# Kernel tuning notes

Hardware: AMD Instinct MI355X
Metric: run time of the kernel (lower is better)

The kernel has to match this reference:

```python
import jax, jax.numpy as jnp
import numpy as np
from math import pi

N_TRAJS, N_RES, N_BINS = 20, 300, 34
DIST_BIN_CENTRES = jnp.asarray(np.array([3.75 + 0.5 * i for i in range(N_BINS)], dtype=np.float32))
SIG = 1.25            # gauss_sigma
K_CB_DIST = 150.0
K_HB_DIST = 5.0
K_HB_GEN = 0.0
K_ANG_HB_GEN = 0.0
W_VIOL_MIN = 3.0      # weight_violate_min
EXP_MIN = 1.0         # pairwise_exponent_min
EXP_MAX = 0.75        # pairwise_exponent_max
HB_CUTOFF = 6.0       # hb_cutoff_gen
CUTOFF = 40.0         # pairwise_force_cutoff


def _norm(d):
    # safe euclidean norm over last axis (avoids NaN grad at exactly 0)
    return jnp.sqrt(jnp.maximum((d * d).sum(axis=-1), 1e-12))


def _safe_pow(x, p):
    pos = x > 0
    return jnp.where(pos, jnp.where(pos, x, 1.0) ** p, 0.0)


def _angle_forces(ba, bc, k, close, true_ang):
    ba_n = _norm(ba)
    bc_n = _norm(bc)
    cosang = jnp.clip((ba * bc).sum(-1) / jnp.clip(ba_n * bc_n, 0.1, 100.0), -1.0 + 1e-6, 1.0 - 1e-6)
    forces = k * close * (jnp.arccos(cosang) - true_ang)
    cr = jnp.cross(ba, bc)
    fa_vec = jnp.cross(-ba, cr)
    fc_vec = jnp.cross(bc, cr)
    fa = forces[..., None] * fa_vec / jnp.maximum(_norm(fa_vec), 0.1)[..., None]
    fc = forces[..., None] * fc_vec / jnp.maximum(_norm(fc_vec), 0.1)[..., None]
    fb = -fa - fc
    return fa, fb, fc


def setup_inputs() -> dict:
    key = jax.random.key(0)
    ks = jax.random.split(key, 9)
    B, R = N_TRAJS, N_RES
    base = jax.random.uniform(ks[0], (B, R, 3), dtype=jnp.float32) * 30.0
    def off(k):
        return base + jax.random.normal(k, (B, R, 3), dtype=jnp.float32)
    coords_N = off(ks[1]); coords_C = off(ks[2]); coords_O = off(ks[3])
    coords_CB = off(ks[4]); coords_H = off(ks[5])
    gaussian_weights = jax.random.normal(ks[6], (R, R, N_BINS), dtype=jnp.float32)
    hb_dists_min = 1.5 + 1.5 * jax.random.uniform(ks[7], (R, R), dtype=jnp.float32)
    hb_dists_max = hb_dists_min + 1.0 + 2.0 * jax.random.uniform(ks[8], (R, R), dtype=jnp.float32)
    return {"coords_N": coords_N, "coords_C": coords_C, "coords_O": coords_O,
            "coords_CB": coords_CB, "coords_H": coords_H,
            "gaussian_weights": gaussian_weights,
            "hb_dists_min": hb_dists_min, "hb_dists_max": hb_dists_max}


def reference(coords_N, coords_C, coords_O, coords_CB, coords_H,
              gaussian_weights, hb_dists_min, hb_dists_max):
    B, R, _ = coords_CB.shape
    idx = jnp.arange(R)
    # mask excluding |i-j| <= 2 (self and near-diagonal), as in the torch diag_mask
    diag_mask = (jnp.abs(idx[:, None] - idx[None, :]) > 2).astype(jnp.float32)[None]

    # --- CB distogram gaussian pairwise forces ---
    diffs_cb = coords_CB[:, None, :, :] - coords_CB[:, :, None, :]   # [B,i,j,3] = cb_j - cb_i
    dists_cb = jnp.clip(_norm(diffs_cb), 0.1, CUTOFF)                 # [B,i,j]
    norm_cb = diffs_cb / dists_cb[..., None]
    dfm = dists_cb[..., None] - DIST_BIN_CENTRES                      # [B,i,j,K]
    cb_e = gaussian_weights[None] * jnp.exp(-0.5 * (dfm / SIG) ** 2) / SIG
    f_cb = (-dfm / (SIG * SIG) * cb_e).sum(axis=3)                    # [B,i,j]
    pair_cb = -f_cb[..., None] * K_CB_DIST * norm_cb
    accs_CB = pair_cb.sum(axis=1)

    # --- H..O hydrogen-bond min/max distance restraints ---
    diffs_ho = coords_O[:, None, :, :] - coords_H[:, :, None, :]      # [B,i,j,3] = o_j - h_i
    dists_ho = jnp.clip(_norm(diffs_ho), 0.1, CUTOFF)
    norm_ho = diffs_ho / dists_ho[..., None]
    v_min = jnp.maximum(hb_dists_min[None] - dists_ho, 0.0)
    v_max = jnp.maximum(dists_ho - hb_dists_max[None], 0.0)
    close = (dists_ho < HB_CUTOFF).astype(jnp.float32) * diag_mask
    v_max_gen = close * jnp.maximum(dists_ho - HB_CUTOFF, 0.0)
    f_min = W_VIOL_MIN * K_HB_DIST * _safe_pow(v_min, EXP_MIN)
    f_max = K_HB_DIST * _safe_pow(v_max, EXP_MAX) + K_HB_GEN * _safe_pow(v_max_gen, EXP_MAX)
    pair_hb = (f_min - f_max)[..., None] * norm_ho
    accs_H = -pair_hb.sum(axis=2)
    accs_O = pair_hb.sum(axis=1)

    # --- O-H-N angle term (k_ang_hb_gen = 0, kept for fidelity) ---
    diffs_hn = (coords_N - coords_H)[:, :, None, :]                   # [B,i,1,3], broadcast over j
    fa, fb, fc = _angle_forces(diffs_ho, diffs_hn, K_ANG_HB_GEN, close, pi)
    accs_O = accs_O + fa.sum(axis=1)
    accs_H = accs_H + fb.sum(axis=2)
    accs_N = fc.sum(axis=2)

    # --- C-O-H angle term ---
    diffs_oc = (coords_C - coords_O)[:, :, None, :]                   # [B,i,1,3]
    fa2, fb2, fc2 = _angle_forces(diffs_oc, -diffs_ho, K_ANG_HB_GEN, close, pi)
    accs_C = fa2.sum(axis=2)
    accs_O = accs_O + fb2.sum(axis=1)
    accs_H = accs_H + fc2.sum(axis=2)

    return (accs_N, accs_C, accs_O, accs_CB, accs_H)
```

## Files before the change

### kernel.cpp

```cpp
#include <hip/hip_runtime.h>

#define NRES  300
#define NTRJ  20
#define NBINS 34
#define PLANE (NTRJ * NRES * 3)
#define IC    2
#define NCH   150
#define NHP   20
#define WROW  544
#define WF2   272
#define NRED  ((PLANE + 255) / 256)

#define EXP2F(x) __builtin_exp2f(x)
#define LOG2F(x) __builtin_log2f(x)

__device__ __forceinline__ float g16sum(float v) {
#pragma unroll
  for (int m = 1; m < 16; m <<= 1) v += __shfl_xor(v, m, 64);
  return v;
}

template <bool PART>
__global__ __launch_bounds__(256)
void force_fused(const float* __restrict__ cO, const float* __restrict__ cCB,
                 const float* __restrict__ cH, const float* __restrict__ gw,
                 const float* __restrict__ hmin, const float* __restrict__ hmax,
                 float* __restrict__ out, float* __restrict__ part) {
  __shared__ float wbuf[4][WROW];
  __shared__ float sCB[NTRJ * IC * 3];
  __shared__ float sHH[NTRJ * IC * 3];

  const int tid  = threadIdx.x;
  const int wv   = tid >> 6;
  const int lane = tid & 63;
  const int bsub = lane >> 4;
  const int jsub = lane & 15;
  const int jt   = blockIdx.x % 5;
  const int ch   = blockIdx.x / 5;
  const int i0   = ch * IC;
  const int j0w  = jt * 64 + wv * 16;
  const int j    = j0w + jsub;
  const bool jv  = (j < NRES);
  const int jc   = jv ? j : NRES - 1;
  const int nrow = min(16, max(0, NRES - j0w));
  const int E2   = nrow * 17;

  for (int e = tid; e < NTRJ * IC * 3; e += 256) {
    const int b = e / (IC * 3), r = e % (IC * 3);
    sCB[e] = cCB[((b * NRES) + i0 + r / 3) * 3 + (r % 3)];
    sHH[e] = cH [((b * NRES) + i0 + r / 3) * 3 + (r % 3)];
  }
  __syncthreads();

  float pjx[5], pjy[5], pjz[5], pox[5], poy[5], poz[5];
  float acx[5] = {}, acy[5] = {}, acz[5] = {};
  float aox[5] = {}, aoy[5] = {}, aoz[5] = {};
#pragma unroll
  for (int q = 0; q < 5; ++q) {
    const int b = bsub * 5 + q;
    const float* p = cCB + ((size_t)(b * NRES + jc)) * 3;
    pjx[q] = p[0]; pjy[q] = p[1]; pjz[q] = p[2];
    const float* o = cO + ((size_t)(b * NRES + jc)) * 3;
    pox[q] = o[0]; poy[q] = o[1]; poz[q] = o[2];
  }

  float2 r2[5];
  {
    const float2* src = (const float2*)gw + ((size_t)i0 * NRES + j0w) * 17;
#pragma unroll
    for (int u = 0; u < 5; ++u) {
      const int e = lane + u * 64;
      r2[u] = (e < E2) ? src[e] : make_float2(0.f, 0.f);
    }
  }

  float2* wd = (float2*)&wbuf[wv][0];
  for (int ii = 0; ii < IC; ++ii) {
    const int i = i0 + ii;
#pragma unroll
    for (int u = 0; u < 5; ++u) {
      const int e = lane + u * 64;
      if (e < WF2) wd[e] = r2[u];
    }
    if (ii + 1 < IC) {
      const float2* src =
          (const float2*)gw + ((size_t)(i + 1) * NRES + j0w) * 17;
#pragma unroll
      for (int u = 0; u < 5; ++u) {
        const int e = lane + u * 64;
        r2[u] = (e < E2) ? src[e] : make_float2(0.f, 0.f);
      }
    }

    float w[36];
    const float2* p2 = (const float2*)&wbuf[wv][jsub * NBINS];
#pragma unroll
    for (int k = 0; k < 17; ++k) { float2 v = p2[k]; w[2*k] = v.x; w[2*k+1] = v.y; }
    w[34] = 0.f; w[35] = 0.f;

    const float hmn = hmin[i * NRES + jc];
    const float hmx = hmax[i * NRES + jc];

#pragma unroll
    for (int q = 0; q < 5; ++q) {
      const int b = bsub * 5 + q;
      const float* pi = &sCB[(b * IC + ii) * 3];
      const float* ph = &sHH[(b * IC + ii) * 3];

      float dx = pjx[q] - pi[0], dy = pjy[q] - pi[1], dz = pjz[q] - pi[2];
      float d2 = fmaf(dx, dx, fmaf(dy, dy, dz * dz));
      d2 = fminf(fmaxf(d2, 0.01f), 1600.0f);
      float rinv = __frsqrt_rn(d2);
      float d    = d2 * rinv;
      float dA = d - 3.75f, dB = d - 9.75f, dC = d - 15.75f;
      float gA = EXP2F(-0.46166241f * dA * dA);
      float mA = EXP2F(fmaf(0.46166241f, dA, -0.11541560f));
      float gB = EXP2F(-0.46166241f * dB * dB);
      float mB = EXP2F(fmaf(0.46166241f, dB, -0.11541560f));
      float gC = EXP2F(-0.46166241f * dC * dC);
      float mC = EXP2F(fmaf(0.46166241f, dC, -0.11541560f));
      float s0 = 0.f, s1 = 0.f, s2 = 0.f;
#pragma unroll
      for (int k = 0; k < 12; ++k) {
        s0 = fmaf(w[k]      * dA, gA, s0); gA *= mA; mA *= 0.85214379f; dA -= 0.5f;
        s1 = fmaf(w[k + 12] * dB, gB, s1); gB *= mB; mB *= 0.85214379f; dB -= 0.5f;
        s2 = fmaf(w[k + 24] * dC, gC, s2); gC *= mC; mC *= 0.85214379f; dC -= 0.5f;
      }
      float cf = 76.8f * ((s0 + s1) + s2) * rinv;
      acx[q] = fmaf(cf, dx, acx[q]);
      acy[q] = fmaf(cf, dy, acy[q]);
      acz[q] = fmaf(cf, dz, acz[q]);

      float ex = pox[q] - ph[0], ey = poy[q] - ph[1], ez = poz[q] - ph[2];
      float e2 = fmaf(ex, ex, fmaf(ey, ey, ez * ez));
      e2 = fminf(fmaxf(e2, 0.01f), 1600.0f);
      float rh = __frsqrt_rn(e2);
      float dh = e2 * rh;
      float vmin = fmaxf(hmn - dh, 0.0f);
      float vmax = fmaxf(dh - hmx, 0.0f);
      float fmn = 15.0f * vmin;
      float fmx = (vmax > 0.0f) ? 5.0f * EXP2F(0.75f * LOG2F(vmax)) : 0.0f;
      float ff = (fmn - fmx) * rh;
      float qx = ff * ex, qy = ff * ey, qz = ff * ez;
      aox[q] += qx; aoy[q] += qy; aoz[q] += qz;

      float sx = g16sum(jv ? qx : 0.f);
      float sy = g16sum(jv ? qy : 0.f);
      float sz = g16sum(jv ? qz : 0.f);
      if (jsub == 0) {
        if constexpr (PART) {
          float* hp = part + ((size_t)(2 * NCH + jt * 4 + wv)) * PLANE +
                      ((size_t)b * NRES + i) * 3;
          hp[0] = -sx; hp[1] = -sy; hp[2] = -sz;
        } else {
          atomicAdd(&out[4 * PLANE + (b * NRES + i) * 3 + 0], -sx);
          atomicAdd(&out[4 * PLANE + (b * NRES + i) * 3 + 1], -sy);
          atomicAdd(&out[4 * PLANE + (b * NRES + i) * 3 + 2], -sz);
        }
      }
    }
  }

  if (jv) {
    if constexpr (PART) {
      float* pc  = part + (size_t)ch * PLANE;
      float* po2 = part + (size_t)(NCH + ch) * PLANE;
#pragma unroll
      for (int q = 0; q < 5; ++q) {
        const int base = ((bsub * 5 + q) * NRES + j) * 3;
        pc[base + 0]  = acx[q]; pc[base + 1]  = acy[q]; pc[base + 2]  = acz[q];
        po2[base + 0] = aox[q]; po2[base + 1] = aoy[q]; po2[base + 2] = aoz[q];
      }
    } else {
#pragma unroll
      for (int q = 0; q < 5; ++q) {
        const int base = ((bsub * 5 + q) * NRES + j) * 3;
        atomicAdd(&out[3 * PLANE + base + 0], acx[q]);
        atomicAdd(&out[3 * PLANE + base + 1], acy[q]);
        atomicAdd(&out[3 * PLANE + base + 2], acz[q]);
        atomicAdd(&out[2 * PLANE + base + 0], aox[q]);
        atomicAdd(&out[2 * PLANE + base + 1], aoy[q]);
        atomicAdd(&out[2 * PLANE + base + 2], aoz[q]);
      }
    }
  }
}

__global__ __launch_bounds__(256)
void reduce_seg(const float* __restrict__ part, float* __restrict__ out) {
  const int seg  = blockIdx.x / NRED;
  const int tblk = blockIdx.x % NRED;
  const int t    = tblk * 256 + threadIdx.x;
  if (t >= PLANE) return;

  int c0, cnt;
  float* dst;
  if (seg < 3)      { c0 = seg * 50;             cnt = 50; dst = out + 3 * PLANE; }
  else if (seg < 6) { c0 = NCH + (seg - 3) * 50; cnt = 50; dst = out + 2 * PLANE; }
  else              { c0 = 2 * NCH;              cnt = 20; dst = out + 4 * PLANE; }

  const float* p = part + t + (size_t)c0 * PLANE;
  float s[10] = {};
  for (int c = 0; c < cnt; c += 10) {
#pragma unroll
    for (int u = 0; u < 10; ++u) s[u] += p[(size_t)(c + u) * PLANE];
  }
  float tot = ((s[0] + s[1]) + (s[2] + s[3])) + ((s[4] + s[5]) + (s[6] + s[7])) +
              (s[8] + s[9]);
  atomicAdd(&dst[t], tot);
}

extern "C" void kernel_launch(void* const* d_in, const int* in_sizes, int n_in,
                              void* d_out, int out_size, void* d_ws, size_t ws_size,
                              hipStream_t stream) {
  const float* cO  = (const float*)d_in[2];
  const float* cCB = (const float*)d_in[3];
  const float* cH  = (const float*)d_in[4];
  const float* gw  = (const float*)d_in[5];
  const float* hmn = (const float*)d_in[6];
  const float* hmx = (const float*)d_in[7];
  float* out  = (float*)d_out;
  float* part = (float*)d_ws;

  const size_t need = (size_t)(2 * NCH + NHP) * PLANE * sizeof(float);

  (void)hipMemsetAsync(out, 0, (size_t)out_size * sizeof(float), stream);

  if (ws_size >= need) {
    force_fused<true><<<dim3(5 * NCH), dim3(256), 0, stream>>>(
        cO, cCB, cH, gw, hmn, hmx, out, part);
    reduce_seg<<<dim3(7 * NRED), dim3(256), 0, stream>>>(part, out);
  } else {
    force_fused<false><<<dim3(5 * NCH), dim3(256), 0, stream>>>(
        cO, cCB, cH, gw, hmn, hmx, out, nullptr);
  }
}
```

Baseline: 39.79 us.

## Split H-force accumulation into dedicated blocks, removing per-pair shuffle reductions

```diff
diff --git a/kernel.cpp b/kernel.cpp
--- a/kernel.cpp
+++ b/kernel.cpp
@@ -6,19 +6,16 @@
 #define PLANE (NTRJ * NRES * 3)
 #define IC    2
 #define NCH   150
-#define NHP   20
-#define WROW  544
-#define WF2   272
+#define NCBB  (5 * NCH)
+#define NHCH  15
+#define NHBB  (5 * NHCH)
+#define OFF_H (2 * NCH)
+#define NPLANES (2 * NCH + NHCH)
+#define WROWP 36
 #define NRED  ((PLANE + 255) / 256)
 
 #define EXP2F(x) __builtin_exp2f(x)
 #define LOG2F(x) __builtin_log2f(x)
-
-__device__ __forceinline__ float g16sum(float v) {
-#pragma unroll
-  for (int m = 1; m < 16; m <<= 1) v += __shfl_xor(v, m, 64);
-  return v;
-}
 
 template <bool PART>
 __global__ __launch_bounds__(256)
@@ -26,65 +23,51 @@
                  const float* __restrict__ cH, const float* __restrict__ gw,
                  const float* __restrict__ hmin, const float* __restrict__ hmax,
                  float* __restrict__ out, float* __restrict__ part) {
-  __shared__ float wbuf[4][WROW];
-  __shared__ float sCB[NTRJ * IC * 3];
-  __shared__ float sHH[NTRJ * IC * 3];
+  __shared__ __align__(16) float smem[3800];
 
   const int tid  = threadIdx.x;
   const int wv   = tid >> 6;
   const int lane = tid & 63;
-  const int bsub = lane >> 4;
-  const int jsub = lane & 15;
-  const int jt   = blockIdx.x % 5;
-  const int ch   = blockIdx.x / 5;
-  const int i0   = ch * IC;
-  const int j0w  = jt * 64 + wv * 16;
-  const int j    = j0w + jsub;
-  const bool jv  = (j < NRES);
-  const int jc   = jv ? j : NRES - 1;
-  const int nrow = min(16, max(0, NRES - j0w));
-  const int E2   = nrow * 17;
-
-  for (int e = tid; e < NTRJ * IC * 3; e += 256) {
-    const int b = e / (IC * 3), r = e % (IC * 3);
-    sCB[e] = cCB[((b * NRES) + i0 + r / 3) * 3 + (r % 3)];
-    sHH[e] = cH [((b * NRES) + i0 + r / 3) * 3 + (r % 3)];
-  }
-  __syncthreads();
-
-  float pjx[5], pjy[5], pjz[5], pox[5], poy[5], poz[5];
-  float acx[5] = {}, acy[5] = {}, acz[5] = {};
-  float aox[5] = {}, aoy[5] = {}, aoz[5] = {};
-#pragma unroll
-  for (int q = 0; q < 5; ++q) {
-    const int b = bsub * 5 + q;
-    const float* p = cCB + ((size_t)(b * NRES + jc)) * 3;
-    pjx[q] = p[0]; pjy[q] = p[1]; pjz[q] = p[2];
-    const float* o = cO + ((size_t)(b * NRES + jc)) * 3;
-    pox[q] = o[0]; poy[q] = o[1]; poz[q] = o[2];
-  }
-
-  float2 r2[5];
-  {
-    const float2* src = (const float2*)gw + ((size_t)i0 * NRES + j0w) * 17;
-#pragma unroll
-    for (int u = 0; u < 5; ++u) {
-      const int e = lane + u * 64;
-      r2[u] = (e < E2) ? src[e] : make_float2(0.f, 0.f);
-    }
-  }
-
-  float2* wd = (float2*)&wbuf[wv][0];
-  for (int ii = 0; ii < IC; ++ii) {
-    const int i = i0 + ii;
-#pragma unroll
-    for (int u = 0; u < 5; ++u) {
-      const int e = lane + u * 64;
-      if (e < WF2) wd[e] = r2[u];
-    }
-    if (ii + 1 < IC) {
-      const float2* src =
-          (const float2*)gw + ((size_t)(i + 1) * NRES + j0w) * 17;
+
+  if (blockIdx.x < NCBB) {
+    float* wbufw = smem + wv * (16 * WROWP);
+    float* sIC   = smem + 4 * (16 * WROWP);
+
+    const int bsub = lane >> 4;
+    const int jsub = lane & 15;
+    const int jt   = blockIdx.x % 5;
+    const int ch   = blockIdx.x / 5;
+    const int i0   = ch * IC;
+    const int j0w  = jt * 64 + wv * 16;
+    const int j    = j0w + jsub;
+    const bool jv  = (j < NRES);
+    const int jc   = jv ? j : NRES - 1;
+    const int E2   = 17 * min(16, max(0, NRES - j0w));
+
+    for (int e = tid; e < NTRJ * IC * 6; e += 256) {
+      const int b = e / (IC * 6), r = e % (IC * 6);
+      const int ii = r / 6, c = r % 6;
+      const int comp = (c < 3) ? c : c - 3;
+      const int src = ((b * NRES) + i0 + ii) * 3 + comp;
+      sIC[(b * IC + ii) * 8 + (c < 3 ? c : c + 1)] = (c < 3) ? cCB[src] : cH[src];
+    }
+    __syncthreads();
+
+    float pjx[5], pjy[5], pjz[5], pox[5], poy[5], poz[5];
+    float acx[5] = {}, acy[5] = {}, acz[5] = {};
+    float aox[5] = {}, aoy[5] = {}, aoz[5] = {};
+#pragma unroll
+    for (int q = 0; q < 5; ++q) {
+      const int b = bsub * 5 + q;
+      const float* p = cCB + ((size_t)(b * NRES + jc)) * 3;
+      pjx[q] = p[0]; pjy[q] = p[1]; pjz[q] = p[2];
+      const float* o = cO + ((size_t)(b * NRES + jc)) * 3;
+      pox[q] = o[0]; poy[q] = o[1]; poz[q] = o[2];
+    }
+
+    float2 r2[5];
+    {
+      const float2* src = (const float2*)gw + ((size_t)i0 * NRES + j0w) * 17;
 #pragma unroll
       for (int u = 0; u < 5; ++u) {
         const int e = lane + u * 64;
@@ -92,95 +75,181 @@
       }
     }
 
-    float w[36];
-    const float2* p2 = (const float2*)&wbuf[wv][jsub * NBINS];
-#pragma unroll
-    for (int k = 0; k < 17; ++k) { float2 v = p2[k]; w[2*k] = v.x; w[2*k+1] = v.y; }
-    w[34] = 0.f; w[35] = 0.f;
-
-    const float hmn = hmin[i * NRES + jc];
-    const float hmx = hmax[i * NRES + jc];
-
+    for (int ii = 0; ii < IC; ++ii) {
+      const int i = i0 + ii;
+#pragma unroll
+      for (int u = 0; u < 5; ++u) {
+        const int e = lane + u * 64;
+        if (e < 272) {
+          const int row = e / 17, col = e - row * 17;
+          ((float2*)wbufw)[row * 18 + col] = r2[u];
+        }
+      }
+      if (ii + 1 < IC) {
+        const float2* src =
+            (const float2*)gw + ((size_t)(i + 1) * NRES + j0w) * 17;
+#pragma unroll
+        for (int u = 0; u < 5; ++u) {
+          const int e = lane + u * 64;
+          r2[u] = (e < E2) ? src[e] : make_float2(0.f, 0.f);
+        }
+      }
+
+      float w[36];
+      {
+        const float4* wp = (const float4*)&wbufw[jsub * WROWP];
+#pragma unroll
+        for (int k4 = 0; k4 < 9; ++k4) {
+          float4 v = wp[k4];
+          w[4*k4+0] = v.x; w[4*k4+1] = v.y; w[4*k4+2] = v.z; w[4*k4+3] = v.w;
+        }
+        w[34] = 0.f; w[35] = 0.f;
+      }
+
+      const float hmn = hmin[i * NRES + jc];
+      const float hmx = hmax[i * NRES + jc];
+
+#pragma unroll
+      for (int q = 0; q < 5; ++q) {
+        const int b = bsub * 5 + q;
+        const float4* ic4 = (const float4*)&sIC[(b * IC + ii) * 8];
+        const float4 cb = ic4[0];
+        const float4 hh = ic4[1];
+
+        float dx = pjx[q] - cb.x, dy = pjy[q] - cb.y, dz = pjz[q] - cb.z;
+        float d2 = fmaf(dx, dx, fmaf(dy, dy, dz * dz));
+        d2 = fminf(fmaxf(d2, 0.01f), 1600.0f);
+        float rinv = __frsqrt_rn(d2);
+        float d    = d2 * rinv;
+        float dA = d - 3.75f, dB = d - 9.75f, dC = d - 15.75f;
+        float gA = EXP2F(-0.46166241f * dA * dA);
+        float mA = EXP2F(fmaf(0.46166241f, dA, -0.11541560f));
+        float gB = EXP2F(-0.46166241f * dB * dB);
+        float mB = EXP2F(fmaf(0.46166241f, dB, -0.11541560f));
+        float gC = EXP2F(-0.46166241f * dC * dC);
+        float mC = EXP2F(fmaf(0.46166241f, dC, -0.11541560f));
+        float s0 = 0.f, s1 = 0.f, s2 = 0.f;
+#pragma unroll
+        for (int k = 0; k < 12; ++k) {
+          s0 = fmaf(w[k]      * dA, gA, s0); gA *= mA; mA *= 0.85214379f; dA -= 0.5f;
+          s1 = fmaf(w[k + 12] * dB, gB, s1); gB *= mB; mB *= 0.85214379f; dB -= 0.5f;
+          s2 = fmaf(w[k + 24] * dC, gC, s2); gC *= mC; mC *= 0.85214379f; dC -= 0.5f;
+        }
+        float cf = 76.8f * ((s0 + s1) + s2) * rinv;
+        acx[q] = fmaf(cf, dx, acx[q]);
+        acy[q] = fmaf(cf, dy, acy[q]);
+        acz[q] = fmaf(cf, dz, acz[q]);
+
+        float ex = pox[q] - hh.x, ey = poy[q] - hh.y, ez = poz[q] - hh.z;
+        float e2 = fmaf(ex, ex, fmaf(ey, ey, ez * ez));
+        e2 = fminf(fmaxf(e2, 0.01f), 1600.0f);
+        float rh = __frsqrt_rn(e2);
+        float dh = e2 * rh;
+        float vmin = fmaxf(hmn - dh, 0.0f);
+        float vmax = fmaxf(dh - hmx, 0.0f);
+        float fmn = 15.0f * vmin;
+        float fmx = (vmax > 0.0f) ? 5.0f * EXP2F(0.75f * LOG2F(vmax)) : 0.0f;
+        float ff = (fmn - fmx) * rh;
+        aox[q] = fmaf(ff, ex, aox[q]);
+        aoy[q] = fmaf(ff, ey, aoy[q]);
+        aoz[q] = fmaf(ff, ez, aoz[q]);
+      }
+    }
+
+    if (jv) {
+      if constexpr (PART) {
+        float* pc  = part + (size_t)ch * PLANE;
+        float* po2 = part + (size_t)(NCH + ch) * PLANE;
+#pragma unroll
+        for (int q = 0; q < 5; ++q) {
+          const int base = ((bsub * 5 + q) * NRES + j) * 3;
+          pc[base + 0]  = acx[q]; pc[base + 1]  = acy[q]; pc[base + 2]  = acz[q];
+          po2[base + 0] = aox[q]; po2[base + 1] = aoy[q]; po2[base + 2] = aoz[q];
+        }
+      } else {
+#pragma unroll
+        for (int q = 0; q < 5; ++q) {
+          const int base = ((bsub * 5 + q) * NRES + j) * 3;
+          atomicAdd(&out[3 * PLANE + base + 0], acx[q]);
+          atomicAdd(&out[3 * PLANE + base + 1], acy[q]);
+          atomicAdd(&out[3 * PLANE + base + 2], acz[q]);
+          atomicAdd(&out[2 * PLANE + base + 0], aox[q]);
+          atomicAdd(&out[2 * PLANE + base + 1], aoy[q]);
+          atomicAdd(&out[2 * PLANE + base + 2], aoz[q]);
+        }
+      }
+    }
+  } else {
+    float* tmn = smem;
+    float* tmx = smem + 1300;
+    float* sO  = smem + 2600;
+
+    const int bx2 = blockIdx.x - NCBB;
+    const int it  = bx2 % 5;
+    const int jch = bx2 / 5;
+    const int j0  = jch * 20;
+    const int i   = it * 64 + lane;
+    const bool iv = (i < NRES);
+    const int icl = iv ? i : NRES - 1;
+    const int b0  = __builtin_amdgcn_readfirstlane(wv) * 5;
+
+    for (int e = tid; e < 64 * 20; e += 256) {
+      const int row = e / 20, col = e - (e / 20) * 20;
+      int ig = it * 64 + row; if (ig > NRES - 1) ig = NRES - 1;
+      tmn[col * 65 + row] = hmin[ig * NRES + j0 + col];
+      tmx[col * 65 + row] = hmax[ig * NRES + j0 + col];
+    }
+    for (int e = tid; e < NTRJ * 20 * 3; e += 256) {
+      const int b = e / 60, r = e % 60;
+      sO[e] = cO[((b * NRES) + j0 + r / 3) * 3 + (r % 3)];
+    }
+
+    float phx[5], phy[5], phz[5];
+    float ahx[5] = {}, ahy[5] = {}, ahz[5] = {};
 #pragma unroll
     for (int q = 0; q < 5; ++q) {
-      const int b = bsub * 5 + q;
-      const float* pi = &sCB[(b * IC + ii) * 3];
-      const float* ph = &sHH[(b * IC + ii) * 3];
-
-      float dx = pjx[q] - pi[0], dy = pjy[q] - pi[1], dz = pjz[q] - pi[2];
-      float d2 = fmaf(dx, dx, fmaf(dy, dy, dz * dz));
-      d2 = fminf(fmaxf(d2, 0.01f), 1600.0f);
-      float rinv = __frsqrt_rn(d2);
-      float d    = d2 * rinv;
-      float dA = d - 3.75f, dB = d - 9.75f, dC = d - 15.75f;
-      float gA = EXP2F(-0.46166241f * dA * dA);
-      float mA = EXP2F(fmaf(0.46166241f, dA, -0.11541560f));
-      float gB = EXP2F(-0.46166241f * dB * dB);
-      float mB = EXP2F(fmaf(0.46166241f, dB, -0.11541560f));
-      float gC = EXP2F(-0.46166241f * dC * dC);
-      float mC = EXP2F(fmaf(0.46166241f, dC, -0.11541560f));
-      float s0 = 0.f, s1 = 0.f, s2 = 0.f;
-#pragma unroll
-      for (int k = 0; k < 12; ++k) {
-        s0 = fmaf(w[k]      * dA, gA, s0); gA *= mA; mA *= 0.85214379f; dA -= 0.5f;
-        s1 = fmaf(w[k + 12] * dB, gB, s1); gB *= mB; mB *= 0.85214379f; dB -= 0.5f;
-        s2 = fmaf(w[k + 24] * dC, gC, s2); gC *= mC; mC *= 0.85214379f; dC -= 0.5f;
-      }
-      float cf = 76.8f * ((s0 + s1) + s2) * rinv;
-      acx[q] = fmaf(cf, dx, acx[q]);
-      acy[q] = fmaf(cf, dy, acy[q]);
-      acz[q] = fmaf(cf, dz, acz[q]);
-
-      float ex = pox[q] - ph[0], ey = poy[q] - ph[1], ez = poz[q] - ph[2];
-      float e2 = fmaf(ex, ex, fmaf(ey, ey, ez * ez));
-      e2 = fminf(fmaxf(e2, 0.01f), 1600.0f);
-      float rh = __frsqrt_rn(e2);
-      float dh = e2 * rh;
-      float vmin = fmaxf(hmn - dh, 0.0f);
-      float vmax = fmaxf(dh - hmx, 0.0f);
-      float fmn = 15.0f * vmin;
-      float fmx = (vmax > 0.0f) ? 5.0f * EXP2F(0.75f * LOG2F(vmax)) : 0.0f;
-      float ff = (fmn - fmx) * rh;
-      float qx = ff * ex, qy = ff * ey, qz = ff * ez;
-      aox[q] += qx; aoy[q] += qy; aoz[q] += qz;
-
-      float sx = g16sum(jv ? qx : 0.f);
-      float sy = g16sum(jv ? qy : 0.f);
-      float sz = g16sum(jv ? qz : 0.f);
-      if (jsub == 0) {
-        if constexpr (PART) {
-          float* hp = part + ((size_t)(2 * NCH + jt * 4 + wv)) * PLANE +
-                      ((size_t)b * NRES + i) * 3;
-          hp[0] = -sx; hp[1] = -sy; hp[2] = -sz;
-        } else {
-          atomicAdd(&out[4 * PLANE + (b * NRES + i) * 3 + 0], -sx);
-          atomicAdd(&out[4 * PLANE + (b * NRES + i) * 3 + 1], -sy);
-          atomicAdd(&out[4 * PLANE + (b * NRES + i) * 3 + 2], -sz);
-        }
-      }
-    }
-  }
-
-  if (jv) {
-    if constexpr (PART) {
-      float* pc  = part + (size_t)ch * PLANE;
-      float* po2 = part + (size_t)(NCH + ch) * PLANE;
+      const float* h = cH + ((size_t)((b0 + q) * NRES + icl)) * 3;
+      phx[q] = h[0]; phy[q] = h[1]; phz[q] = h[2];
+    }
+    __syncthreads();
+
+    for (int jj = 0; jj < 20; ++jj) {
+      const float hmn = tmn[jj * 65 + lane];
+      const float hmx = tmx[jj * 65 + lane];
 #pragma unroll
       for (int q = 0; q < 5; ++q) {
-        const int base = ((bsub * 5 + q) * NRES + j) * 3;
-        pc[base + 0]  = acx[q]; pc[base + 1]  = acy[q]; pc[base + 2]  = acz[q];
-        po2[base + 0] = aox[q]; po2[base + 1] = aoy[q]; po2[base + 2] = aoz[q];
-      }
-    } else {
-#pragma unroll
-      for (int q = 0; q < 5; ++q) {
-        const int base = ((bsub * 5 + q) * NRES + j) * 3;
-        atomicAdd(&out[3 * PLANE + base + 0], acx[q]);
-        atomicAdd(&out[3 * PLANE + base + 1], acy[q]);
-        atomicAdd(&out[3 * PLANE + base + 2], acz[q]);
-        atomicAdd(&out[2 * PLANE + base + 0], aox[q]);
-        atomicAdd(&out[2 * PLANE + base + 1], aoy[q]);
-        atomicAdd(&out[2 * PLANE + base + 2], aoz[q]);
+        const float* po = &sO[((b0 + q) * 20 + jj) * 3];
+        float ex = po[0] - phx[q], ey = po[1] - phy[q], ez = po[2] - phz[q];
+        float e2 = fmaf(ex, ex, fmaf(ey, ey, ez * ez));
+        e2 = fminf(fmaxf(e2, 0.01f), 1600.0f);
+        float rh = __frsqrt_rn(e2);
+        float dh = e2 * rh;
+        float vmin = fmaxf(hmn - dh, 0.0f);
+        float vmax = fmaxf(dh - hmx, 0.0f);
+        float fmn = 15.0f * vmin;
+        float fmx = (vmax > 0.0f) ? 5.0f * EXP2F(0.75f * LOG2F(vmax)) : 0.0f;
+        float ff = (fmn - fmx) * rh;
+        ahx[q] = fmaf(-ff, ex, ahx[q]);
+        ahy[q] = fmaf(-ff, ey, ahy[q]);
+        ahz[q] = fmaf(-ff, ez, ahz[q]);
+      }
+    }
+    if (iv) {
+      if constexpr (PART) {
+        float* hp = part + (size_t)(OFF_H + jch) * PLANE;
+#pragma unroll
+        for (int q = 0; q < 5; ++q) {
+          const int base = ((b0 + q) * NRES + i) * 3;
+          hp[base + 0] = ahx[q]; hp[base + 1] = ahy[q]; hp[base + 2] = ahz[q];
+        }
+      } else {
+#pragma unroll
+        for (int q = 0; q < 5; ++q) {
+          const int base = ((b0 + q) * NRES + i) * 3;
+          atomicAdd(&out[4 * PLANE + base + 0], ahx[q]);
+          atomicAdd(&out[4 * PLANE + base + 1], ahy[q]);
+          atomicAdd(&out[4 * PLANE + base + 2], ahz[q]);
+        }
       }
     }
   }
@@ -189,25 +258,24 @@
 __global__ __launch_bounds__(256)
 void reduce_seg(const float* __restrict__ part, float* __restrict__ out) {
   const int seg  = blockIdx.x / NRED;
-  const int tblk = blockIdx.x % NRED;
-  const int t    = tblk * 256 + threadIdx.x;
+  const int t    = (blockIdx.x % NRED) * 256 + threadIdx.x;
   if (t >= PLANE) return;
 
   int c0, cnt;
-  float* dst;
-  if (seg < 3)      { c0 = seg * 50;             cnt = 50; dst = out + 3 * PLANE; }
-  else if (seg < 6) { c0 = NCH + (seg - 3) * 50; cnt = 50; dst = out + 2 * PLANE; }
-  else              { c0 = 2 * NCH;              cnt = 20; dst = out + 4 * PLANE; }
+  if (seg < 3)      { c0 = seg * 50;             cnt = 50; }
+  else if (seg < 6) { c0 = NCH + (seg - 3) * 50; cnt = 50; }
+  else              { c0 = OFF_H;                cnt = NHCH; }
 
   const float* p = part + t + (size_t)c0 * PLANE;
-  float s[10] = {};
-  for (int c = 0; c < cnt; c += 10) {
-#pragma unroll
-    for (int u = 0; u < 10; ++u) s[u] += p[(size_t)(c + u) * PLANE];
+  float s[5] = {};
+  for (int c = 0; c < cnt; c += 5) {
+#pragma unroll
+    for (int u = 0; u < 5; ++u) s[u] += p[(size_t)(c + u) * PLANE];
   }
-  float tot = ((s[0] + s[1]) + (s[2] + s[3])) + ((s[4] + s[5]) + (s[6] + s[7])) +
-              (s[8] + s[9]);
-  atomicAdd(&dst[t], tot);
+  const float tot = ((s[0] + s[1]) + (s[2] + s[3])) + s[4];
+  if (seg < 3)      atomicAdd(&out[3 * PLANE + t], tot);
+  else if (seg < 6) atomicAdd(&out[2 * PLANE + t], tot);
+  else              out[4 * PLANE + t] = tot;
 }
 
 extern "C" void kernel_launch(void* const* d_in, const int* in_sizes, int n_in,
@@ -222,16 +290,14 @@
   float* out  = (float*)d_out;
   float* part = (float*)d_ws;
 
-  const size_t need = (size_t)(2 * NCH + NHP) * PLANE * sizeof(float);
-
   (void)hipMemsetAsync(out, 0, (size_t)out_size * sizeof(float), stream);
 
-  if (ws_size >= need) {
-    force_fused<true><<<dim3(5 * NCH), dim3(256), 0, stream>>>(
+  if (ws_size >= (size_t)NPLANES * PLANE * sizeof(float)) {
+    force_fused<true><<<dim3(NCBB + NHBB), dim3(256), 0, stream>>>(
         cO, cCB, cH, gw, hmn, hmx, out, part);
     reduce_seg<<<dim3(7 * NRED), dim3(256), 0, stream>>>(part, out);
   } else {
-    force_fused<false><<<dim3(5 * NCH), dim3(256), 0, stream>>>(
+    force_fused<false><<<dim3(NCBB + NHBB), dim3(256), 0, stream>>>(
         cO, cCB, cH, gw, hmn, hmx, out, nullptr);
   }
 }
```

Result: slower. 41.54 us (+4.4%).

## Process one i-row per block and atomically accumulate into fewer partial planes

Applied to the files above, without the earlier changes.

```diff
diff --git a/kernel.cpp b/kernel.cpp
--- a/kernel.cpp
+++ b/kernel.cpp
@@ -4,11 +4,8 @@
 #define NTRJ  20
 #define NBINS 34
 #define PLANE (NTRJ * NRES * 3)
-#define IC    2
-#define NCH   150
-#define NHP   20
-#define WROW  544
-#define WF2   272
+#define NPP   75
+#define OFF_H 150
 #define NRED  ((PLANE + 255) / 256)
 
 #define EXP2F(x) __builtin_exp2f(x)
@@ -26,9 +23,9 @@
                  const float* __restrict__ cH, const float* __restrict__ gw,
                  const float* __restrict__ hmin, const float* __restrict__ hmax,
                  float* __restrict__ out, float* __restrict__ part) {
-  __shared__ float wbuf[4][WROW];
-  __shared__ float sCB[NTRJ * IC * 3];
-  __shared__ float sHH[NTRJ * IC * 3];
+  __shared__ __align__(16) float wlds[4][16 * 36];
+  __shared__ float sIC[NTRJ * 4];
+  __shared__ float sHH[NTRJ * 4];
 
   const int tid  = threadIdx.x;
   const int wv   = tid >> 6;
@@ -36,25 +33,21 @@
   const int bsub = lane >> 4;
   const int jsub = lane & 15;
   const int jt   = blockIdx.x % 5;
-  const int ch   = blockIdx.x / 5;
-  const int i0   = ch * IC;
+  const int i    = blockIdx.x / 5;
   const int j0w  = jt * 64 + wv * 16;
   const int j    = j0w + jsub;
   const bool jv  = (j < NRES);
   const int jc   = jv ? j : NRES - 1;
-  const int nrow = min(16, max(0, NRES - j0w));
-  const int E2   = nrow * 17;
-
-  for (int e = tid; e < NTRJ * IC * 3; e += 256) {
-    const int b = e / (IC * 3), r = e % (IC * 3);
-    sCB[e] = cCB[((b * NRES) + i0 + r / 3) * 3 + (r % 3)];
-    sHH[e] = cH [((b * NRES) + i0 + r / 3) * 3 + (r % 3)];
+  const int E2   = 17 * min(16, max(0, NRES - j0w));
+
+  if (tid < NTRJ * 3) {
+    const int b = tid / 3, c = tid % 3;
+    sIC[b * 4 + c] = cCB[(b * NRES + i) * 3 + c];
+    sHH[b * 4 + c] = cH [(b * NRES + i) * 3 + c];
   }
   __syncthreads();
 
   float pjx[5], pjy[5], pjz[5], pox[5], poy[5], poz[5];
-  float acx[5] = {}, acy[5] = {}, acz[5] = {};
-  float aox[5] = {}, aoy[5] = {}, aoz[5] = {};
 #pragma unroll
   for (int q = 0; q < 5; ++q) {
     const int b = bsub * 5 + q;
@@ -66,110 +59,111 @@
 
   float2 r2[5];
   {
-    const float2* src = (const float2*)gw + ((size_t)i0 * NRES + j0w) * 17;
+    const float2* src = (const float2*)gw + ((size_t)i * NRES + j0w) * 17;
 #pragma unroll
     for (int u = 0; u < 5; ++u) {
       const int e = lane + u * 64;
       r2[u] = (e < E2) ? src[e] : make_float2(0.f, 0.f);
     }
   }
-
-  float2* wd = (float2*)&wbuf[wv][0];
-  for (int ii = 0; ii < IC; ++ii) {
-    const int i = i0 + ii;
+  {
+    float2* wd = (float2*)&wlds[wv][0];
 #pragma unroll
     for (int u = 0; u < 5; ++u) {
       const int e = lane + u * 64;
-      if (e < WF2) wd[e] = r2[u];
-    }
-    if (ii + 1 < IC) {
-      const float2* src =
-          (const float2*)gw + ((size_t)(i + 1) * NRES + j0w) * 17;
-#pragma unroll
-      for (int u = 0; u < 5; ++u) {
-        const int e = lane + u * 64;
-        r2[u] = (e < E2) ? src[e] : make_float2(0.f, 0.f);
-      }
-    }
-
-    float w[36];
-    const float2* p2 = (const float2*)&wbuf[wv][jsub * NBINS];
-#pragma unroll
-    for (int k = 0; k < 17; ++k) { float2 v = p2[k]; w[2*k] = v.x; w[2*k+1] = v.y; }
+      if (e < 272) {
+        const int row = e / 17, col = e - row * 17;
+        wd[row * 18 + col] = r2[u];
+      }
+    }
+  }
+
+  float w[36];
+  {
+    const float4* wp = (const float4*)&wlds[wv][jsub * 36];
+#pragma unroll
+    for (int k4 = 0; k4 < 9; ++k4) {
+      float4 v = wp[k4];
+      w[4*k4+0] = v.x; w[4*k4+1] = v.y; w[4*k4+2] = v.z; w[4*k4+3] = v.w;
+    }
     w[34] = 0.f; w[35] = 0.f;
-
-    const float hmn = hmin[i * NRES + jc];
-    const float hmx = hmax[i * NRES + jc];
-
-#pragma unroll
-    for (int q = 0; q < 5; ++q) {
-      const int b = bsub * 5 + q;
-      const float* pi = &sCB[(b * IC + ii) * 3];
-      const float* ph = &sHH[(b * IC + ii) * 3];
-
-      float dx = pjx[q] - pi[0], dy = pjy[q] - pi[1], dz = pjz[q] - pi[2];
-      float d2 = fmaf(dx, dx, fmaf(dy, dy, dz * dz));
-      d2 = fminf(fmaxf(d2, 0.01f), 1600.0f);
-      float rinv = __frsqrt_rn(d2);
-      float d    = d2 * rinv;
-      float dA = d - 3.75f, dB = d - 9.75f, dC = d - 15.75f;
-      float gA = EXP2F(-0.46166241f * dA * dA);
-      float mA = EXP2F(fmaf(0.46166241f, dA, -0.11541560f));
-      float gB = EXP2F(-0.46166241f * dB * dB);
-      float mB = EXP2F(fmaf(0.46166241f, dB, -0.11541560f));
-      float gC = EXP2F(-0.46166241f * dC * dC);
-      float mC = EXP2F(fmaf(0.46166241f, dC, -0.11541560f));
-      float s0 = 0.f, s1 = 0.f, s2 = 0.f;
-#pragma unroll
-      for (int k = 0; k < 12; ++k) {
-        s0 = fmaf(w[k]      * dA, gA, s0); gA *= mA; mA *= 0.85214379f; dA -= 0.5f;
-        s1 = fmaf(w[k + 12] * dB, gB, s1); gB *= mB; mB *= 0.85214379f; dB -= 0.5f;
-        s2 = fmaf(w[k + 24] * dC, gC, s2); gC *= mC; mC *= 0.85214379f; dC -= 0.5f;
-      }
-      float cf = 76.8f * ((s0 + s1) + s2) * rinv;
-      acx[q] = fmaf(cf, dx, acx[q]);
-      acy[q] = fmaf(cf, dy, acy[q]);
-      acz[q] = fmaf(cf, dz, acz[q]);
-
-      float ex = pox[q] - ph[0], ey = poy[q] - ph[1], ez = poz[q] - ph[2];
-      float e2 = fmaf(ex, ex, fmaf(ey, ey, ez * ez));
-      e2 = fminf(fmaxf(e2, 0.01f), 1600.0f);
-      float rh = __frsqrt_rn(e2);
-      float dh = e2 * rh;
-      float vmin = fmaxf(hmn - dh, 0.0f);
-      float vmax = fmaxf(dh - hmx, 0.0f);
-      float fmn = 15.0f * vmin;
-      float fmx = (vmax > 0.0f) ? 5.0f * EXP2F(0.75f * LOG2F(vmax)) : 0.0f;
-      float ff = (fmn - fmx) * rh;
-      float qx = ff * ex, qy = ff * ey, qz = ff * ez;
-      aox[q] += qx; aoy[q] += qy; aoz[q] += qz;
-
-      float sx = g16sum(jv ? qx : 0.f);
-      float sy = g16sum(jv ? qy : 0.f);
-      float sz = g16sum(jv ? qz : 0.f);
-      if (jsub == 0) {
-        if constexpr (PART) {
-          float* hp = part + ((size_t)(2 * NCH + jt * 4 + wv)) * PLANE +
-                      ((size_t)b * NRES + i) * 3;
-          hp[0] = -sx; hp[1] = -sy; hp[2] = -sz;
-        } else {
-          atomicAdd(&out[4 * PLANE + (b * NRES + i) * 3 + 0], -sx);
-          atomicAdd(&out[4 * PLANE + (b * NRES + i) * 3 + 1], -sy);
-          atomicAdd(&out[4 * PLANE + (b * NRES + i) * 3 + 2], -sz);
-        }
+  }
+
+  const float hmn = hmin[i * NRES + jc];
+  const float hmx = hmax[i * NRES + jc];
+
+  float acx[5], acy[5], acz[5], aox[5], aoy[5], aoz[5];
+
+#pragma unroll
+  for (int q = 0; q < 5; ++q) {
+    const int b = bsub * 5 + q;
+    const float* pi = &sIC[b * 4];
+    const float* ph = &sHH[b * 4];
+
+    float dx = pjx[q] - pi[0], dy = pjy[q] - pi[1], dz = pjz[q] - pi[2];
+    float d2 = fmaf(dx, dx, fmaf(dy, dy, dz * dz));
+    d2 = fminf(fmaxf(d2, 0.01f), 1600.0f);
+    float rinv = __frsqrt_rn(d2);
+    float d    = d2 * rinv;
+    float dA = d - 3.75f, dB = d - 9.75f, dC = d - 15.75f;
+    float gA = EXP2F(-0.46166241f * dA * dA);
+    float gB = EXP2F(-0.46166241f * dB * dB);
+    float gC = EXP2F(-0.46166241f * dC * dC);
+    float mA = EXP2F(fmaf(0.46166241f, dA, -0.11541560f));
+    float mB = mA * 0.14660697f;
+    float mC = mA * 0.02149329f;
+    float s0 = 0.f, s1 = 0.f, s2 = 0.f;
+#pragma unroll
+    for (int k = 0; k < 12; ++k) {
+      s0 = fmaf(w[k]      * dA, gA, s0); gA *= mA; mA *= 0.85214379f; dA -= 0.5f;
+      s1 = fmaf(w[k + 12] * dB, gB, s1); gB *= mB; mB *= 0.85214379f; dB -= 0.5f;
+      s2 = fmaf(w[k + 24] * dC, gC, s2); gC *= mC; mC *= 0.85214379f; dC -= 0.5f;
+    }
+    float cf = 76.8f * ((s0 + s1) + s2) * rinv;
+    acx[q] = cf * dx; acy[q] = cf * dy; acz[q] = cf * dz;
+
+    float ex = pox[q] - ph[0], ey = poy[q] - ph[1], ez = poz[q] - ph[2];
+    float e2 = fmaf(ex, ex, fmaf(ey, ey, ez * ez));
+    e2 = fminf(fmaxf(e2, 0.01f), 1600.0f);
+    float rh = __frsqrt_rn(e2);
+    float dh = e2 * rh;
+    float vmin = fmaxf(hmn - dh, 0.0f);
+    float vmax = fmaxf(dh - hmx, 0.0f);
+    float fmn = 15.0f * vmin;
+    float fmx = (vmax > 0.0f) ? 5.0f * EXP2F(0.75f * LOG2F(vmax)) : 0.0f;
+    float ff = (fmn - fmx) * rh;
+    float qx = ff * ex, qy = ff * ey, qz = ff * ez;
+    aox[q] = qx; aoy[q] = qy; aoz[q] = qz;
+
+    float sx = g16sum(jv ? qx : 0.f);
+    float sy = g16sum(jv ? qy : 0.f);
+    float sz = g16sum(jv ? qz : 0.f);
+    if (jsub == 0) {
+      if constexpr (PART) {
+        float* hp = part + (size_t)(OFF_H + jt * 4 + wv) * PLANE +
+                    ((size_t)b * NRES + i) * 3;
+        hp[0] = -sx; hp[1] = -sy; hp[2] = -sz;
+      } else {
+        atomicAdd(&out[4 * PLANE + (b * NRES + i) * 3 + 0], -sx);
+        atomicAdd(&out[4 * PLANE + (b * NRES + i) * 3 + 1], -sy);
+        atomicAdd(&out[4 * PLANE + (b * NRES + i) * 3 + 2], -sz);
       }
     }
   }
 
   if (jv) {
     if constexpr (PART) {
-      float* pc  = part + (size_t)ch * PLANE;
-      float* po2 = part + (size_t)(NCH + ch) * PLANE;
+      float* pc  = part + (size_t)(i % NPP) * PLANE;
+      float* po2 = part + (size_t)(NPP + i % NPP) * PLANE;
 #pragma unroll
       for (int q = 0; q < 5; ++q) {
         const int base = ((bsub * 5 + q) * NRES + j) * 3;
-        pc[base + 0]  = acx[q]; pc[base + 1]  = acy[q]; pc[base + 2]  = acz[q];
-        po2[base + 0] = aox[q]; po2[base + 1] = aoy[q]; po2[base + 2] = aoz[q];
+        atomicAdd(&pc[base + 0],  acx[q]);
+        atomicAdd(&pc[base + 1],  acy[q]);
+        atomicAdd(&pc[base + 2],  acz[q]);
+        atomicAdd(&po2[base + 0], aox[q]);
+        atomicAdd(&po2[base + 1], aoy[q]);
+        atomicAdd(&po2[base + 2], aoz[q]);
       }
     } else {
 #pragma unroll
@@ -188,26 +182,31 @@
 
 __global__ __launch_bounds__(256)
 void reduce_seg(const float* __restrict__ part, float* __restrict__ out) {
-  const int seg  = blockIdx.x / NRED;
-  const int tblk = blockIdx.x % NRED;
-  const int t    = tblk * 256 + threadIdx.x;
+  const int seg = blockIdx.x / NRED;
+  const int t   = (blockIdx.x % NRED) * 256 + threadIdx.x;
   if (t >= PLANE) return;
 
-  int c0, cnt;
-  float* dst;
-  if (seg < 3)      { c0 = seg * 50;             cnt = 50; dst = out + 3 * PLANE; }
-  else if (seg < 6) { c0 = NCH + (seg - 3) * 50; cnt = 50; dst = out + 2 * PLANE; }
-  else              { c0 = 2 * NCH;              cnt = 20; dst = out + 4 * PLANE; }
-
-  const float* p = part + t + (size_t)c0 * PLANE;
-  float s[10] = {};
-  for (int c = 0; c < cnt; c += 10) {
-#pragma unroll
-    for (int u = 0; u < 10; ++u) s[u] += p[(size_t)(c + u) * PLANE];
-  }
-  float tot = ((s[0] + s[1]) + (s[2] + s[3])) + ((s[4] + s[5]) + (s[6] + s[7])) +
-              (s[8] + s[9]);
-  atomicAdd(&dst[t], tot);
+  if (seg < 6) {
+    const int c0 = (seg < 3) ? seg * 25 : NPP + (seg - 3) * 25;
+    const float* p = part + t + (size_t)c0 * PLANE;
+    float s[5] = {};
+#pragma unroll
+    for (int c = 0; c < 25; c += 5) {
+#pragma unroll
+      for (int u = 0; u < 5; ++u) s[u] += p[(size_t)(c + u) * PLANE];
+    }
+    const float tot = ((s[0] + s[1]) + (s[2] + s[3])) + s[4];
+    atomicAdd(&out[((seg < 3) ? 3 : 2) * PLANE + t], tot);
+  } else {
+    const float* p = part + t + (size_t)OFF_H * PLANE;
+    float s[5] = {};
+#pragma unroll
+    for (int c = 0; c < 20; c += 5) {
+#pragma unroll
+      for (int u = 0; u < 5; ++u) s[u] += p[(size_t)(c + u) * PLANE];
+    }
+    out[4 * PLANE + t] = ((s[0] + s[1]) + (s[2] + s[3])) + s[4];
+  }
 }
 
 extern "C" void kernel_launch(void* const* d_in, const int* in_sizes, int n_in,
@@ -222,16 +221,17 @@
   float* out  = (float*)d_out;
   float* part = (float*)d_ws;
 
-  const size_t need = (size_t)(2 * NCH + NHP) * PLANE * sizeof(float);
+  const size_t need = (size_t)(OFF_H + 20) * PLANE * sizeof(float);
 
   (void)hipMemsetAsync(out, 0, (size_t)out_size * sizeof(float), stream);
 
   if (ws_size >= need) {
-    force_fused<true><<<dim3(5 * NCH), dim3(256), 0, stream>>>(
+    (void)hipMemsetAsync(part, 0, (size_t)2 * NPP * PLANE * sizeof(float), stream);
+    force_fused<true><<<dim3(5 * NRES), dim3(256), 0, stream>>>(
         cO, cCB, cH, gw, hmn, hmx, out, part);
     reduce_seg<<<dim3(7 * NRED), dim3(256), 0, stream>>>(part, out);
   } else {
-    force_fused<false><<<dim3(5 * NCH), dim3(256), 0, stream>>>(
+    force_fused<false><<<dim3(5 * NRES), dim3(256), 0, stream>>>(
         cO, cCB, cH, gw, hmn, hmx, out, nullptr);
   }
 }
```

Result: slower. 152.9 us (+284.2%).
